# Kernel tuning notes

Measured on AMD Instinct MI355X. Metric: run time of the kernel, lower is better.

## Reference

```python
import jax, jax.numpy as jnp
import numpy as np

HIDDEN = 4096
INTER = 11008
BATCH, SEQ = 2, 2048


def _ternary(key, shape):
    # BitNet b1.58 ternary weights in {-1, 0, +1}
    return jax.random.randint(key, shape, -1, 2).astype(jnp.float32)


def setup_inputs() -> dict:
    key = jax.random.key(0)
    kx, kg, ku, kd = jax.random.split(key, 4)
    x = jax.random.normal(kx, (BATCH, SEQ, HIDDEN), dtype=jnp.float32)
    gate_w = _ternary(kg, (INTER, HIDDEN))
    up_w = _ternary(ku, (INTER, HIDDEN))
    down_w = _ternary(kd, (HIDDEN, INTER))
    # per-tensor absmean scales (dequant factors)
    gate_scale = jnp.float32(0.02)
    up_scale = jnp.float32(0.02)
    down_scale = jnp.float32(0.02)
    return {"x": x, "gate_w": gate_w, "up_w": up_w, "down_w": down_w,
            "gate_scale": gate_scale, "up_scale": up_scale, "down_scale": down_scale}


def reference(x, gate_w, up_w, down_w, gate_scale, up_scale, down_scale):
    # QuantizedLinear: y = (x @ W_q^T) * scale, W_q ternary, bias=False
    gate = jnp.einsum('bsh,ih->bsi', x, gate_w) * gate_scale
    up = jnp.einsum('bsh,ih->bsi', x, up_w) * up_scale
    inter = jax.nn.silu(gate) * up  # SwiGLU
    out = jnp.einsum('bsi,hi->bsh', inter, down_w) * down_scale
    return out
```

## Files before the change

### kernel.cpp

```cpp
#include <hip/hip_runtime.h>


typedef short short8 __attribute__((ext_vector_type(8)));
typedef float f32x4 __attribute__((ext_vector_type(4)));
typedef float fvec4 __attribute__((ext_vector_type(4)));
typedef unsigned short usvec4 __attribute__((ext_vector_type(4)));

#define BM 128
#define BK 32

__device__ __forceinline__ unsigned short f2bf(float f) {
    unsigned int u = __float_as_uint(f);
    u += 0x7FFFu + ((u >> 16) & 1u);
    return (unsigned short)(u >> 16);
}

__global__ void cvt_f32_bf16(const fvec4* __restrict__ src,
                             usvec4* __restrict__ dst, long n4) {
    long i = (long)blockIdx.x * blockDim.x + threadIdx.x;
    if (i < n4) {
        fvec4 v = __builtin_nontemporal_load(src + i);
        usvec4 o;
        o.x = f2bf(v.x); o.y = f2bf(v.y); o.z = f2bf(v.z); o.w = f2bf(v.w);
        dst[i] = o;
    }
}

__global__ void cvt2_f32_bf16(const fvec4* __restrict__ s0,
                              const fvec4* __restrict__ s1,
                              usvec4* __restrict__ d0,
                              usvec4* __restrict__ d1, long n4) {
    long i = (long)blockIdx.x * blockDim.x + threadIdx.x;
    if (i < n4) {
        fvec4 a = __builtin_nontemporal_load(s0 + i);
        fvec4 b = __builtin_nontemporal_load(s1 + i);
        usvec4 oa, ob;
        oa.x = f2bf(a.x); oa.y = f2bf(a.y); oa.z = f2bf(a.z); oa.w = f2bf(a.w);
        ob.x = f2bf(b.x); ob.y = f2bf(b.y); ob.z = f2bf(b.z); ob.w = f2bf(b.w);
        d0[i] = oa;
        d1[i] = ob;
    }
}

#define GLOBAL_TO_LDS(gp, lp)                                                  \
    __builtin_amdgcn_global_load_lds(                                          \
        (__attribute__((address_space(1))) const void*)(gp),                   \
        (__attribute__((address_space(3))) void*)(lp), 16, 0, 0)

__global__ __launch_bounds__(256, 2)
void gemm1_swiglu(const unsigned short* __restrict__ Xb,
                  const unsigned short* __restrict__ Gw,
                  const unsigned short* __restrict__ Uw,
                  unsigned short* __restrict__ inter,
                  const float* __restrict__ gs_p,
                  const float* __restrict__ us_p,
                  int K, int I, int n0) {
    __shared__ unsigned short As[BM * BK];
    __shared__ unsigned short Bg[BM * BK];
    __shared__ unsigned short Bu[BM * BK];

    const int tid = threadIdx.x;
    const int m_base = blockIdx.x * BM;
    const int nb = blockIdx.y * BM;

    f32x4 accg[4][4], accu[4][4];
    const f32x4 z = {0.0f, 0.0f, 0.0f, 0.0f};
#pragma unroll
    for (int i = 0; i < 4; ++i)
#pragma unroll
        for (int j = 0; j < 4; ++j) { accg[i][j] = z; accu[i][j] = z; }

    const int lane = tid & 63;
    const int wid = tid >> 6;
    const int wm = (wid >> 1) * 64;
    const int wn = (wid & 1) * 64;
    const int fr = lane & 15;

    const int c0 = tid, c1 = tid + 256;
    const int r0 = c0 >> 2, r1 = c1 >> 2;
    const int kc0 = (((c0 & 3) ^ ((c0 >> 3) & 3)) << 3);
    const int kc1 = (((c1 & 3) ^ ((c1 >> 3) & 3)) << 3);
    const int ca = (((lane >> 4) ^ ((fr >> 1) & 3)) << 3);

    for (int k0 = 0; k0 < K; k0 += BK) {
        GLOBAL_TO_LDS(Xb + (size_t)(m_base + r0) * K + (k0 + kc0), &As[c0 * 8]);
        GLOBAL_TO_LDS(Xb + (size_t)(m_base + r1) * K + (k0 + kc1), &As[c1 * 8]);
        GLOBAL_TO_LDS(Gw + (size_t)(nb + r0) * K + (k0 + kc0), &Bg[c0 * 8]);
        GLOBAL_TO_LDS(Gw + (size_t)(nb + r1) * K + (k0 + kc1), &Bg[c1 * 8]);
        GLOBAL_TO_LDS(Uw + (size_t)(nb + r0) * K + (k0 + kc0), &Bu[c0 * 8]);
        GLOBAL_TO_LDS(Uw + (size_t)(nb + r1) * K + (k0 + kc1), &Bu[c1 * 8]);
        __syncthreads();

        short8 a[4], bg[4], bu[4];
#pragma unroll
        for (int i = 0; i < 4; ++i) {
            a[i]  = *(const short8*)(&As[(wm + i * 16 + fr) * BK + ca]);
            bg[i] = *(const short8*)(&Bg[(wn + i * 16 + fr) * BK + ca]);
            bu[i] = *(const short8*)(&Bu[(wn + i * 16 + fr) * BK + ca]);
        }
#pragma unroll
        for (int mi = 0; mi < 4; ++mi)
#pragma unroll
            for (int ni = 0; ni < 4; ++ni) {
                accg[mi][ni] = __builtin_amdgcn_mfma_f32_16x16x32_bf16(
                    a[mi], bg[ni], accg[mi][ni], 0, 0, 0);
                accu[mi][ni] = __builtin_amdgcn_mfma_f32_16x16x32_bf16(
                    a[mi], bu[ni], accu[mi][ni], 0, 0, 0);
            }
        __syncthreads();
    }

    const float gsc = *gs_p;
    const float usc = *us_p;
    const int row0 = m_base + wm + (lane >> 4) * 4;
    const int col0 = n0 + nb + wn + fr;
#pragma unroll
    for (int mi = 0; mi < 4; ++mi)
#pragma unroll
        for (int ni = 0; ni < 4; ++ni)
#pragma unroll
            for (int r = 0; r < 4; ++r) {
                float g = accg[mi][ni][r] * gsc;
                float u = accu[mi][ni][r] * usc;
                float s = g / (1.0f + __expf(-g));
                inter[(size_t)(row0 + mi * 16 + r) * I + (col0 + ni * 16)] =
                    f2bf(s * u);
            }
}

__global__ __launch_bounds__(256, 2)
void gemm2_down(const unsigned short* __restrict__ Ab,
                const unsigned short* __restrict__ Dw,
                float* __restrict__ out,
                const float* __restrict__ ds_p,
                int K, int H, int n0) {
    __shared__ unsigned short As[BM * BK];
    __shared__ unsigned short B0[BM * BK];
    __shared__ unsigned short B1[BM * BK];

    const int tid = threadIdx.x;
    const int m_base = blockIdx.x * BM;
    const int nb = blockIdx.y * 256;

    f32x4 acc0[4][4], acc1[4][4];
    const f32x4 z = {0.0f, 0.0f, 0.0f, 0.0f};
#pragma unroll
    for (int i = 0; i < 4; ++i)
#pragma unroll
        for (int j = 0; j < 4; ++j) { acc0[i][j] = z; acc1[i][j] = z; }

    const int lane = tid & 63;
    const int wid = tid >> 6;
    const int wm = (wid >> 1) * 64;
    const int wn = (wid & 1) * 64;
    const int fr = lane & 15;

    const int c0 = tid, c1 = tid + 256;
    const int r0 = c0 >> 2, r1 = c1 >> 2;
    const int kc0 = (((c0 & 3) ^ ((c0 >> 3) & 3)) << 3);
    const int kc1 = (((c1 & 3) ^ ((c1 >> 3) & 3)) << 3);
    const int ca = (((lane >> 4) ^ ((fr >> 1) & 3)) << 3);

    const unsigned short* D0 = Dw + (size_t)nb * K;
    const unsigned short* D1 = Dw + (size_t)(nb + BM) * K;

    for (int k0 = 0; k0 < K; k0 += BK) {
        GLOBAL_TO_LDS(Ab + (size_t)(m_base + r0) * K + (k0 + kc0), &As[c0 * 8]);
        GLOBAL_TO_LDS(Ab + (size_t)(m_base + r1) * K + (k0 + kc1), &As[c1 * 8]);
        GLOBAL_TO_LDS(D0 + (size_t)r0 * K + (k0 + kc0), &B0[c0 * 8]);
        GLOBAL_TO_LDS(D0 + (size_t)r1 * K + (k0 + kc1), &B0[c1 * 8]);
        GLOBAL_TO_LDS(D1 + (size_t)r0 * K + (k0 + kc0), &B1[c0 * 8]);
        GLOBAL_TO_LDS(D1 + (size_t)r1 * K + (k0 + kc1), &B1[c1 * 8]);
        __syncthreads();

        short8 a[4], b0[4], b1[4];
#pragma unroll
        for (int i = 0; i < 4; ++i) {
            a[i]  = *(const short8*)(&As[(wm + i * 16 + fr) * BK + ca]);
            b0[i] = *(const short8*)(&B0[(wn + i * 16 + fr) * BK + ca]);
            b1[i] = *(const short8*)(&B1[(wn + i * 16 + fr) * BK + ca]);
        }
#pragma unroll
        for (int mi = 0; mi < 4; ++mi)
#pragma unroll
            for (int ni = 0; ni < 4; ++ni) {
                acc0[mi][ni] = __builtin_amdgcn_mfma_f32_16x16x32_bf16(
                    a[mi], b0[ni], acc0[mi][ni], 0, 0, 0);
                acc1[mi][ni] = __builtin_amdgcn_mfma_f32_16x16x32_bf16(
                    a[mi], b1[ni], acc1[mi][ni], 0, 0, 0);
            }
        __syncthreads();
    }

    const float dsc = *ds_p;
    const int row0 = m_base + wm + (lane >> 4) * 4;
    const int colA = n0 + nb + wn + fr;
    const int colB = colA + BM;
#pragma unroll
    for (int mi = 0; mi < 4; ++mi)
#pragma unroll
        for (int ni = 0; ni < 4; ++ni)
#pragma unroll
            for (int r = 0; r < 4; ++r) {
                const size_t rowoff = (size_t)(row0 + mi * 16 + r) * H;
                out[rowoff + (colA + ni * 16)] = acc0[mi][ni][r] * dsc;
                out[rowoff + (colB + ni * 16)] = acc1[mi][ni][r] * dsc;
            }
}

extern "C" void kernel_launch(void* const* d_in, const int* in_sizes, int n_in,
                              void* d_out, int out_size, void* d_ws, size_t ws_size,
                              hipStream_t stream) {
    (void)in_sizes; (void)n_in; (void)out_size;
    const float* x  = (const float*)d_in[0];
    const float* gw = (const float*)d_in[1];
    const float* uw = (const float*)d_in[2];
    const float* dw = (const float*)d_in[3];
    const float* gs = (const float*)d_in[4];
    const float* us = (const float*)d_in[5];
    const float* ds = (const float*)d_in[6];
    float* out = (float*)d_out;

    const long M = 4096;
    const long Kh = 4096;
    const long I = 11008;
    const long H = 4096;

    char* ws = (char*)d_ws;
    unsigned short* Xb = (unsigned short*)ws;
    unsigned short* inter = (unsigned short*)(ws + M * Kh * 2);
    const size_t used = (size_t)M * Kh * 2 + (size_t)M * I * 2;
    if (ws_size < used + 2 * (size_t)256 * I * 2) return;
    char* wbuf = ws + used;
    const size_t avail = ws_size - used;

    {
        long n4 = M * Kh / 4;
        cvt_f32_bf16<<<dim3((unsigned)((n4 + 255) / 256)), dim3(256), 0, stream>>>(
            (const fvec4*)x, (usvec4*)Xb, n4);
    }

    long mr1 = (long)(avail / ((size_t)2 * Kh * 2));
    mr1 = (mr1 / 128) * 128;
    if (mr1 > 5504) mr1 = 5504;
    if (mr1 < 128) mr1 = 128;
    unsigned short* Wg = (unsigned short*)wbuf;
    unsigned short* Wu = (unsigned short*)(wbuf + (size_t)mr1 * Kh * 2);
    for (long n0 = 0; n0 < I; n0 += mr1) {
        long rc = (I - n0 < mr1) ? (I - n0) : mr1;
        long e4 = rc * Kh / 4;
        unsigned cb = (unsigned)((e4 + 255) / 256);
        cvt2_f32_bf16<<<dim3(cb), dim3(256), 0, stream>>>(
            (const fvec4*)(gw + n0 * Kh), (const fvec4*)(uw + n0 * Kh),
            (usvec4*)Wg, (usvec4*)Wu, e4);
        gemm1_swiglu<<<dim3((unsigned)(M / BM), (unsigned)(rc / BM)), dim3(256), 0, stream>>>(
            Xb, Wg, Wu, inter, gs, us, (int)Kh, (int)I, (int)n0);
    }

    long mr2 = (long)(avail / ((size_t)I * 2));
    mr2 = (mr2 / 256) * 256;
    if (mr2 > H) mr2 = H;
    if (mr2 < 256) mr2 = 256;
    unsigned short* Wd = (unsigned short*)wbuf;
    for (long h0 = 0; h0 < H; h0 += mr2) {
        long rc = (H - h0 < mr2) ? (H - h0) : mr2;
        long e4 = rc * I / 4;
        unsigned cb = (unsigned)((e4 + 255) / 256);
        cvt_f32_bf16<<<dim3(cb), dim3(256), 0, stream>>>(
            (const fvec4*)(dw + h0 * I), (usvec4*)Wd, e4);
        gemm2_down<<<dim3((unsigned)(M / BM), (unsigned)(rc / 256)), dim3(256), 0, stream>>>(
            inter, Wd, out, ds, (int)I, (int)H, (int)h0);
    }
}
```

Before: 1.611 ms.

## Fuse fp32-to-bf16 weight conversion into GEMM tile staging

Drops the separate weight conversion kernels and the chunked launch loops. Both GEMMs now read fp32 weights directly, pack them to bf16 in registers by truncation (byte permute), and write them to LDS instead of using async global-to-LDS loads. This avoids writing and re-reading converted weight buffers, but every tile now loads twice as many bytes of weight data, through synchronous register loads with no overlap. The rounding also changes from round-to-nearest-even to truncation, which is exact for ternary weights.

```diff
diff --git a/kernel.cpp b/kernel.cpp
--- a/kernel.cpp
+++ b/kernel.cpp
@@ -5,6 +5,7 @@
 typedef float f32x4 __attribute__((ext_vector_type(4)));
 typedef float fvec4 __attribute__((ext_vector_type(4)));
 typedef unsigned short usvec4 __attribute__((ext_vector_type(4)));
+typedef unsigned int u32x4 __attribute__((ext_vector_type(4)));
 
 #define BM 128
 #define BK 32
@@ -26,20 +27,15 @@
     }
 }
 
-__global__ void cvt2_f32_bf16(const fvec4* __restrict__ s0,
-                              const fvec4* __restrict__ s1,
-                              usvec4* __restrict__ d0,
-                              usvec4* __restrict__ d1, long n4) {
-    long i = (long)blockIdx.x * blockDim.x + threadIdx.x;
-    if (i < n4) {
-        fvec4 a = __builtin_nontemporal_load(s0 + i);
-        fvec4 b = __builtin_nontemporal_load(s1 + i);
-        usvec4 oa, ob;
-        oa.x = f2bf(a.x); oa.y = f2bf(a.y); oa.z = f2bf(a.z); oa.w = f2bf(a.w);
-        ob.x = f2bf(b.x); ob.y = f2bf(b.y); ob.z = f2bf(b.z); ob.w = f2bf(b.w);
-        d0[i] = oa;
-        d1[i] = ob;
-    }
+__device__ __forceinline__ u32x4 pack_bf16x8(fvec4 a, fvec4 b) {
+    union { fvec4 f; u32x4 u; } ua, ub;
+    ua.f = a; ub.f = b;
+    u32x4 r;
+    r.x = __builtin_amdgcn_perm(ua.u.y, ua.u.x, 0x07060302u);
+    r.y = __builtin_amdgcn_perm(ua.u.w, ua.u.z, 0x07060302u);
+    r.z = __builtin_amdgcn_perm(ub.u.y, ub.u.x, 0x07060302u);
+    r.w = __builtin_amdgcn_perm(ub.u.w, ub.u.z, 0x07060302u);
+    return r;
 }
 
 #define GLOBAL_TO_LDS(gp, lp)                                                  \
@@ -47,14 +43,24 @@
         (__attribute__((address_space(1))) const void*)(gp),                   \
         (__attribute__((address_space(3))) void*)(lp), 16, 0, 0)
 
+#define STAGE_W_TILE(Wf, lds)                                                  \
+    do {                                                                       \
+        const float* p0_ = (Wf) + (size_t)r0 * K + (k0 + kc0);                 \
+        const float* p1_ = (Wf) + (size_t)r1 * K + (k0 + kc1);                 \
+        fvec4 a0_ = *(const fvec4*)p0_, a1_ = *(const fvec4*)(p0_ + 4);        \
+        fvec4 b0_ = *(const fvec4*)p1_, b1_ = *(const fvec4*)(p1_ + 4);        \
+        *(u32x4*)(&(lds)[c0 * 8]) = pack_bf16x8(a0_, a1_);                     \
+        *(u32x4*)(&(lds)[c1 * 8]) = pack_bf16x8(b0_, b1_);                     \
+    } while (0)
+
 __global__ __launch_bounds__(256, 2)
 void gemm1_swiglu(const unsigned short* __restrict__ Xb,
-                  const unsigned short* __restrict__ Gw,
-                  const unsigned short* __restrict__ Uw,
+                  const float* __restrict__ Gw,
+                  const float* __restrict__ Uw,
                   unsigned short* __restrict__ inter,
                   const float* __restrict__ gs_p,
                   const float* __restrict__ us_p,
-                  int K, int I, int n0) {
+                  int K, int I) {
     __shared__ unsigned short As[BM * BK];
     __shared__ unsigned short Bg[BM * BK];
     __shared__ unsigned short Bu[BM * BK];
@@ -82,13 +88,14 @@
     const int kc1 = (((c1 & 3) ^ ((c1 >> 3) & 3)) << 3);
     const int ca = (((lane >> 4) ^ ((fr >> 1) & 3)) << 3);
 
+    const float* Gt = Gw + (size_t)nb * K;
+    const float* Ut = Uw + (size_t)nb * K;
+
     for (int k0 = 0; k0 < K; k0 += BK) {
         GLOBAL_TO_LDS(Xb + (size_t)(m_base + r0) * K + (k0 + kc0), &As[c0 * 8]);
         GLOBAL_TO_LDS(Xb + (size_t)(m_base + r1) * K + (k0 + kc1), &As[c1 * 8]);
-        GLOBAL_TO_LDS(Gw + (size_t)(nb + r0) * K + (k0 + kc0), &Bg[c0 * 8]);
-        GLOBAL_TO_LDS(Gw + (size_t)(nb + r1) * K + (k0 + kc1), &Bg[c1 * 8]);
-        GLOBAL_TO_LDS(Uw + (size_t)(nb + r0) * K + (k0 + kc0), &Bu[c0 * 8]);
-        GLOBAL_TO_LDS(Uw + (size_t)(nb + r1) * K + (k0 + kc1), &Bu[c1 * 8]);
+        STAGE_W_TILE(Gt, Bg);
+        STAGE_W_TILE(Ut, Bu);
         __syncthreads();
 
         short8 a[4], bg[4], bu[4];
@@ -113,7 +120,7 @@
     const float gsc = *gs_p;
     const float usc = *us_p;
     const int row0 = m_base + wm + (lane >> 4) * 4;
-    const int col0 = n0 + nb + wn + fr;
+    const int col0 = nb + wn + fr;
 #pragma unroll
     for (int mi = 0; mi < 4; ++mi)
 #pragma unroll
@@ -130,10 +137,10 @@
 
 __global__ __launch_bounds__(256, 2)
 void gemm2_down(const unsigned short* __restrict__ Ab,
-                const unsigned short* __restrict__ Dw,
+                const float* __restrict__ Dw,
                 float* __restrict__ out,
                 const float* __restrict__ ds_p,
-                int K, int H, int n0) {
+                int K, int H) {
     __shared__ unsigned short As[BM * BK];
     __shared__ unsigned short B0[BM * BK];
     __shared__ unsigned short B1[BM * BK];
@@ -161,16 +168,14 @@
     const int kc1 = (((c1 & 3) ^ ((c1 >> 3) & 3)) << 3);
     const int ca = (((lane >> 4) ^ ((fr >> 1) & 3)) << 3);
 
-    const unsigned short* D0 = Dw + (size_t)nb * K;
-    const unsigned short* D1 = Dw + (size_t)(nb + BM) * K;
+    const float* D0 = Dw + (size_t)nb * K;
+    const float* D1 = Dw + (size_t)(nb + BM) * K;
 
     for (int k0 = 0; k0 < K; k0 += BK) {
         GLOBAL_TO_LDS(Ab + (size_t)(m_base + r0) * K + (k0 + kc0), &As[c0 * 8]);
         GLOBAL_TO_LDS(Ab + (size_t)(m_base + r1) * K + (k0 + kc1), &As[c1 * 8]);
-        GLOBAL_TO_LDS(D0 + (size_t)r0 * K + (k0 + kc0), &B0[c0 * 8]);
-        GLOBAL_TO_LDS(D0 + (size_t)r1 * K + (k0 + kc1), &B0[c1 * 8]);
-        GLOBAL_TO_LDS(D1 + (size_t)r0 * K + (k0 + kc0), &B1[c0 * 8]);
-        GLOBAL_TO_LDS(D1 + (size_t)r1 * K + (k0 + kc1), &B1[c1 * 8]);
+        STAGE_W_TILE(D0, B0);
+        STAGE_W_TILE(D1, B1);
         __syncthreads();
 
         short8 a[4], b0[4], b1[4];
@@ -194,7 +199,7 @@
 
     const float dsc = *ds_p;
     const int row0 = m_base + wm + (lane >> 4) * 4;
-    const int colA = n0 + nb + wn + fr;
+    const int colA = nb + wn + fr;
     const int colB = colA + BM;
 #pragma unroll
     for (int mi = 0; mi < 4; ++mi)
@@ -230,9 +235,7 @@
     unsigned short* Xb = (unsigned short*)ws;
     unsigned short* inter = (unsigned short*)(ws + M * Kh * 2);
     const size_t used = (size_t)M * Kh * 2 + (size_t)M * I * 2;
-    if (ws_size < used + 2 * (size_t)256 * I * 2) return;
-    char* wbuf = ws + used;
-    const size_t avail = ws_size - used;
+    if (ws_size < used) return;
 
     {
         long n4 = M * Kh / 4;
@@ -240,35 +243,9 @@
             (const fvec4*)x, (usvec4*)Xb, n4);
     }
 
-    long mr1 = (long)(avail / ((size_t)2 * Kh * 2));
-    mr1 = (mr1 / 128) * 128;
-    if (mr1 > 5504) mr1 = 5504;
-    if (mr1 < 128) mr1 = 128;
-    unsigned short* Wg = (unsigned short*)wbuf;
-    unsigned short* Wu = (unsigned short*)(wbuf + (size_t)mr1 * Kh * 2);
-    for (long n0 = 0; n0 < I; n0 += mr1) {
-        long rc = (I - n0 < mr1) ? (I - n0) : mr1;
-        long e4 = rc * Kh / 4;
-        unsigned cb = (unsigned)((e4 + 255) / 256);
-        cvt2_f32_bf16<<<dim3(cb), dim3(256), 0, stream>>>(
-            (const fvec4*)(gw + n0 * Kh), (const fvec4*)(uw + n0 * Kh),
-            (usvec4*)Wg, (usvec4*)Wu, e4);
-        gemm1_swiglu<<<dim3((unsigned)(M / BM), (unsigned)(rc / BM)), dim3(256), 0, stream>>>(
-            Xb, Wg, Wu, inter, gs, us, (int)Kh, (int)I, (int)n0);
-    }
-
-    long mr2 = (long)(avail / ((size_t)I * 2));
-    mr2 = (mr2 / 256) * 256;
-    if (mr2 > H) mr2 = H;
-    if (mr2 < 256) mr2 = 256;
-    unsigned short* Wd = (unsigned short*)wbuf;
-    for (long h0 = 0; h0 < H; h0 += mr2) {
-        long rc = (H - h0 < mr2) ? (H - h0) : mr2;
-        long e4 = rc * I / 4;
-        unsigned cb = (unsigned)((e4 + 255) / 256);
-        cvt_f32_bf16<<<dim3(cb), dim3(256), 0, stream>>>(
-            (const fvec4*)(dw + h0 * I), (usvec4*)Wd, e4);
-        gemm2_down<<<dim3((unsigned)(M / BM), (unsigned)(rc / 256)), dim3(256), 0, stream>>>(
-            inter, Wd, out, ds, (int)I, (int)H, (int)h0);
-    }
-}
+    gemm1_swiglu<<<dim3((unsigned)(M / BM), (unsigned)(I / BM)), dim3(256), 0, stream>>>(
+        Xb, gw, uw, inter, gs, us, (int)Kh, (int)I);
+
+    gemm2_down<<<dim3((unsigned)(M / BM), (unsigned)(H / 256)), dim3(256), 0, stream>>>(
+        inter, dw, out, ds, (int)I, (int)H);
+}
```

Result: slower. 2.067 ms (+28.3%).
